# Kernel tuning notes

Measured on AMD Instinct MI355X. Metric: run time of the kernel, lower is better.

The kernel has to match this reference:

```python
import jax, jax.numpy as jnp
import numpy as np

B, L, DM, H, M = 4, 2048, 1024, 16, 256
D = DM // H
CHUNK = 128  # chunk size for exact chunked causal linear attention
KERNEL_EPS = 1e-4
NORM_STAB = 1e-6


def setup_inputs() -> dict:
    key = jax.random.key(0)
    ks = jax.random.split(key, 12)
    n = lambda k, shape, s=1.0: jax.random.normal(k, shape, jnp.float32) * s
    w = DM ** -0.5
    return {
        "q": n(ks[0], (B, L, DM)),
        "k": n(ks[1], (B, L, DM)),
        "v": n(ks[2], (B, L, DM)),
        "Wq": n(ks[3], (DM, DM), w), "bq": n(ks[4], (DM,), 0.01),
        "Wk": n(ks[5], (DM, DM), w), "bk": n(ks[6], (DM,), 0.01),
        "Wv": n(ks[7], (DM, DM), w), "bv": n(ks[8], (DM,), 0.01),
        "Wo": n(ks[9], (DM, DM), w), "bo": n(ks[10], (DM,), 0.01),
        "random_features": n(ks[11], (D, M)),  # projection matrix per head-dim
    }


def performer_forward(q, k, v, Wq, bq, Wk, bk, Wv, bv, Wo, bo, random_features):
    b, l, dm = q.shape
    d, m = random_features.shape
    h = dm // d

    def heads(x, W, bias):
        return (x @ W + bias).reshape(b, l, h, d).transpose(0, 2, 1, 3)  # b h l d

    qh, kh, vh = heads(q, Wq, bq), heads(k, Wk, bk), heads(v, Wv, bv)

    scale = dm ** 0.25
    qs, ksc = qh / scale, kh / scale
    pq = jnp.einsum('bhld,dm->bhlm', qs, random_features)
    pk = jnp.einsum('bhld,dm->bhlm', ksc, random_features)
    hk = -0.5 * jnp.sum(ksc * ksc, axis=-1, keepdims=True)
    k_stab = jnp.max(hk)
    c = m ** -0.5
    # q_stabilizer == h_of_q elementwise (last dim is size 1), so exp(h_q + pq - h_q) = exp(pq)
    qp = c * (jnp.exp(pq) + KERNEL_EPS)                 # b h l m
    kp = c * (jnp.exp(hk + pk - k_stab) + KERNEL_EPS)   # b h l m

    # Exact chunked causal linear attention == cumsum of k'(x)v outer products.
    C = CHUNK
    N = l // C
    qc = qp.reshape(b, h, N, C, m)
    kc = kp.reshape(b, h, N, C, m)
    vc = vh.reshape(b, h, N, C, d)
    tril = jnp.tril(jnp.ones((C, C), dtype=qp.dtype))
    A = jnp.einsum('bhnim,bhnjm->bhnij', qc, kc) * tril           # intra-chunk causal scores
    Ssum = jnp.einsum('bhnjm,bhnjd->bhnmd', kc, vc)               # per-chunk sum of k'(x)v
    Sprev = jnp.cumsum(Ssum, axis=2) - Ssum                       # exclusive prefix over chunks
    num = (jnp.einsum('bhnij,bhnjd->bhnid', A, vc)
           + jnp.einsum('bhnim,bhnmd->bhnid', qc, Sprev))         # b h n C d
    zsum = kc.sum(axis=3)                                         # b h n m
    zprev = jnp.cumsum(zsum, axis=2) - zsum
    den = A.sum(axis=-1) + jnp.einsum('bhnim,bhnm->bhni', qc, zprev)
    den = den + 2.0 * NORM_STAB * (jnp.abs(den) <= NORM_STAB).astype(den.dtype)

    out = (num / den[..., None]).reshape(b, h, l, d)
    ctx = out.transpose(0, 2, 1, 3).reshape(b, l, dm)             # b l (h d)
    return ctx @ Wo + bo


def reference(q, k, v, Wq, bq, Wk, bk, Wv, bv, Wo, bo, random_features):
    return performer_forward(q, k, v, Wq, bq, Wk, bk, Wv, bv, Wo, bo, random_features)
```

## Files before the change

kernel.cpp:

```cpp
#include <hip/hip_runtime.h>


typedef unsigned short u16;
typedef unsigned int u32;
typedef __attribute__((ext_vector_type(8))) short bf16x8;
typedef __attribute__((ext_vector_type(4))) float f32x4;

#define MFMA(a, b, c) __builtin_amdgcn_mfma_f32_16x16x32_bf16(a, b, c, 0, 0, 0)
#define WS_NEED 95420416ull

__device__ __forceinline__ float bf2f(u16 u) { return __uint_as_float(((u32)u) << 16); }
__device__ __forceinline__ u16 f2bf(float f) {
  u32 i = __float_as_uint(f);
  u32 r = i + 0x7FFFu + ((i >> 16) & 1u);
  return (u16)(r >> 16);
}
__device__ __forceinline__ u32 fkey(float x) {
  u32 b = __float_as_uint(x);
  return (b & 0x80000000u) ? ~b : (b | 0x80000000u);
}
__device__ __forceinline__ float unfkey(u32 k) {
  return (k & 0x80000000u) ? __uint_as_float(k & 0x7FFFFFFFu) : __uint_as_float(~k);
}
__device__ __forceinline__ uint4 pack_u16x8(const u16 s[8]) {
  uint4 q;
  q.x = (u32)s[0] | ((u32)s[1] << 16);
  q.y = (u32)s[2] | ((u32)s[3] << 16);
  q.z = (u32)s[4] | ((u32)s[5] << 16);
  q.w = (u32)s[6] | ((u32)s[7] << 16);
  return q;
}
__device__ __forceinline__ void gl_lds16(const u16* g, u16* l) {
  __builtin_amdgcn_global_load_lds((const __attribute__((address_space(1))) unsigned int*)g,
                                   (__attribute__((address_space(3))) unsigned int*)l, 16, 0, 0);
}

__global__ __launch_bounds__(256) void k_cast(const float* __restrict__ src,
                                              u16* __restrict__ dst, int n8) {
  int idx = blockIdx.x * 256 + threadIdx.x;
  if (idx >= n8) return;
  const float4* s = (const float4*)src;
  float4 t0 = s[(size_t)idx * 2], t1 = s[(size_t)idx * 2 + 1];
  u16 p[8] = {f2bf(t0.x), f2bf(t0.y), f2bf(t0.z), f2bf(t0.w),
              f2bf(t1.x), f2bf(t1.y), f2bf(t1.z), f2bf(t1.w)};
  *(uint4*)&dst[(size_t)idx * 8] = pack_u16x8(p);
}

__global__ __launch_bounds__(256) void k_transpose(const float* __restrict__ src,
                                                   u16* __restrict__ dst, int R, int C) {
  __shared__ u16 t[64 * 65];
  int r0 = blockIdx.y * 64, c0 = blockIdx.x * 64;
  for (int i = threadIdx.x; i < 4096; i += 256) {
    int rr = i >> 6, cc = i & 63;
    t[rr * 65 + cc] = f2bf(src[(size_t)(r0 + rr) * C + c0 + cc]);
  }
  __syncthreads();
  for (int i = threadIdx.x; i < 4096; i += 256) {
    int cc = i >> 6, rr = i & 63;
    dst[(size_t)(c0 + cc) * R + r0 + rr] = t[rr * 65 + cc];
  }
}

__global__ void k_init(u32* kstab) { *kstab = fkey(-1e30f); }

__global__ __launch_bounds__(256) void k_guard(float* __restrict__ out, size_t ws_size, int n) {
  if (ws_size >= WS_NEED) return;
  int idx = blockIdx.x * 256 + threadIdx.x;
  if (idx < n) out[idx] = 10000.0f + (float)(ws_size >> 20);
}

__global__ __launch_bounds__(256) void k_proj(const void* __restrict__ X,
                                              const u16* __restrict__ WT,
                                              const float* __restrict__ bias,
                                              void* __restrict__ dst, float* __restrict__ HK,
                                              u32* __restrict__ kstab, int mode) {
  __shared__ __align__(16) u16 As[128 * 64];
  __shared__ __align__(16) u16 Bs[128 * 64];
  const int tid = threadIdx.x;
  const int w = tid >> 6, lane = tid & 63, quad = lane >> 4, l15 = lane & 15;
  const int wr = w >> 1, wc = w & 1;
  const int row0 = blockIdx.y * 128;
  const int n0 = blockIdx.x * 128;
  const int lr = lane >> 3;
  const int sub = lane & 7;
  const int colo = ((sub ^ lr) << 3);
  const u16* Xb = (const u16*)X;
  const int bb3 = row0 >> 11, l03 = row0 & 2047;
  f32x4 acc[4][4] = {};
  for (int kb = 0; kb < 1024; kb += 64) {
    __syncthreads();
#pragma unroll
    for (int i = 0; i < 4; ++i)
      gl_lds16(&WT[(size_t)(n0 + w * 32 + i * 8 + lr) * 1024 + kb + colo],
               &Bs[(w * 4 + i) * 512]);
    if (mode <= 2) {
#pragma unroll
      for (int i = 0; i < 4; ++i)
        gl_lds16(&Xb[(size_t)(row0 + w * 32 + i * 8 + lr) * 1024 + kb + colo],
                 &As[(w * 4 + i) * 512]);
    } else {
      const int hh = kb >> 6;
#pragma unroll
      for (int i = 0; i < 4; ++i)
        gl_lds16(&Xb[(((size_t)bb3 * 16 + hh) * 2048 + l03 + w * 32 + i * 8 + lr) * 64 + colo],
                 &As[(w * 4 + i) * 512]);
    }
    __syncthreads();
#pragma unroll
    for (int kk = 0; kk < 2; ++kk) {
      const int s2 = ((kk * 4 + quad) ^ (l15 & 7)) << 3;
      bf16x8 a[4], b[4];
#pragma unroll
      for (int rt = 0; rt < 4; ++rt)
        a[rt] = *(const bf16x8*)&As[(wr * 64 + rt * 16 + l15) * 64 + s2];
#pragma unroll
      for (int ct = 0; ct < 4; ++ct)
        b[ct] = *(const bf16x8*)&Bs[(wc * 64 + ct * 16 + l15) * 64 + s2];
#pragma unroll
      for (int rt = 0; rt < 4; ++rt)
#pragma unroll
        for (int ct = 0; ct < 4; ++ct) acc[rt][ct] = MFMA(a[rt], b[ct], acc[rt][ct]);
    }
  }
  const float sinv = 0.17677669529663687f;
  const int h = blockIdx.x * 2 + wc;
  float sq[4][4] = {};
#pragma unroll
  for (int rt = 0; rt < 4; ++rt)
#pragma unroll
    for (int ct = 0; ct < 4; ++ct) {
      int col = wc * 64 + ct * 16 + l15;
      float bv = bias[n0 + col];
#pragma unroll
      for (int r = 0; r < 4; ++r) {
        int gr = row0 + wr * 64 + rt * 16 + quad * 4 + r;
        float vv = acc[rt][ct][r] + bv;
        if (mode <= 1) vv *= sinv;
        if (mode == 1) sq[rt][r] += vv * vv;
        if (mode == 3) {
          ((float*)dst)[(size_t)gr * 1024 + n0 + col] = vv;
        } else {
          int bb = gr >> 11, ll = gr & 2047;
          ((u16*)dst)[(((size_t)bb * 16 + h) * 2048 + ll) * 64 + ct * 16 + l15] = f2bf(vv);
        }
      }
    }
  if (mode == 1) {
    float mx = -3.4e38f;
#pragma unroll
    for (int rt = 0; rt < 4; ++rt)
#pragma unroll
      for (int r = 0; r < 4; ++r) {
        float s = sq[rt][r];
        s += __shfl_xor(s, 1);
        s += __shfl_xor(s, 2);
        s += __shfl_xor(s, 4);
        s += __shfl_xor(s, 8);
        float hkv = -0.5f * s;
        if (l15 == 0) {
          int gr = row0 + wr * 64 + rt * 16 + quad * 4 + r;
          int bb = gr >> 11, ll = gr & 2047;
          HK[((size_t)bb * 16 + h) * 2048 + ll] = hkv;
        }
        mx = fmaxf(mx, hkv);
      }
    mx = fmaxf(mx, __shfl_xor(mx, 16));
    mx = fmaxf(mx, __shfl_xor(mx, 32));
    if (lane == 0) atomicMax(kstab, fkey(mx));
  }
}

__global__ __launch_bounds__(256) void k_chunksum(const u16* __restrict__ KS,
                                                  const u16* __restrict__ VH,
                                                  const u16* __restrict__ RFt,
                                                  const float* __restrict__ HK,
                                                  const u32* __restrict__ kstab,
                                                  u16* __restrict__ SS,
                                                  float* __restrict__ ZS) {
  __shared__ __align__(16) u16 smem[22784];
  float* hk_l = (float*)&smem[22016];
  float* zpart = (float*)&smem[22272];
  const int tid = threadIdx.x;
  const int w = tid >> 6, lane = tid & 63, quad = lane >> 4, l15 = lane & 15;
  const int bhn = blockIdx.x, bh = bhn >> 4, n = bhn & 15;
  const u16* kc = KS + (size_t)bhn * 8192;
  const u16* vc = VH + (size_t)bhn * 8192;
  const float kst = unfkey(*kstab);
#pragma unroll
  for (int i = 0; i < 4; ++i) {
    int v = tid + i * 256;
    int rr = v >> 3, c8 = (v & 7) << 3;
    *(uint4*)&smem[rr * 72 + c8] = *(const uint4*)&kc[(size_t)rr * 64 + c8];
  }
  {
    int d = tid & 63, jg = tid >> 6;
#pragma unroll
    for (int g = 0; g < 4; ++g) {
      int j0 = jg * 32 + g * 8;
      u16 s[8];
#pragma unroll
      for (int e = 0; e < 8; ++e) s[e] = vc[(size_t)(j0 + e) * 64 + d];
      *(uint4*)&smem[13312 + d * 136 + j0] = pack_u16x8(s);
    }
  }
  if (tid < 128) hk_l[tid] = HK[(size_t)bh * 2048 + n * 128 + tid];
  __syncthreads();
  bf16x8 ak[2][2];
#pragma unroll
  for (int rt = 0; rt < 2; ++rt)
#pragma unroll
    for (int kk = 0; kk < 2; ++kk)
      ak[rt][kk] = *(const bf16x8*)&smem[(w * 32 + rt * 16 + l15) * 72 + kk * 32 + quad * 8];
  for (int mfb = 0; mfb < 4; ++mfb) {
    __syncthreads();
#pragma unroll
    for (int i = 0; i < 2; ++i) {
      int v = tid + i * 256;
      int rr = v >> 3, c8 = (v & 7) << 3;
      *(uint4*)&smem[rr * 72 + c8] = *(const uint4*)&RFt[(size_t)(mfb * 64 + rr) * 64 + c8];
    }
    __syncthreads();
    f32x4 fk[2][4] = {};
#pragma unroll
    for (int kk = 0; kk < 2; ++kk) {
      bf16x8 rb[4];
#pragma unroll
      for (int ct = 0; ct < 4; ++ct)
        rb[ct] = *(const bf16x8*)&smem[(ct * 16 + l15) * 72 + kk * 32 + quad * 8];
#pragma unroll
      for (int rt = 0; rt < 2; ++rt)
#pragma unroll
        for (int ct = 0; ct < 4; ++ct) fk[rt][ct] = MFMA(ak[rt][kk], rb[ct], fk[rt][ct]);
    }
    float zp4[4] = {0.f, 0.f, 0.f, 0.f};
#pragma unroll
    for (int rt = 0; rt < 2; ++rt)
#pragma unroll
      for (int ct = 0; ct < 4; ++ct) {
        int ml = ct * 16 + l15;
#pragma unroll
        for (int r = 0; r < 4; ++r) {
          int j = w * 32 + rt * 16 + quad * 4 + r;
          float kv = 0.0625f * (expf(fminf(hk_l[j] + fk[rt][ct][r] - kst, 80.f)) + 1e-4f);
          smem[4608 + ml * 136 + j] = f2bf(kv);
          zp4[ct] += kv;
        }
      }
#pragma unroll
    for (int ct = 0; ct < 4; ++ct) {
      float s = zp4[ct];
      s += __shfl_xor(s, 16);
      s += __shfl_xor(s, 32);
      if (quad == 0) zpart[w * 64 + ct * 16 + l15] = s;
    }
    __syncthreads();
    f32x4 acc[4] = {};
#pragma unroll
    for (int kk4 = 0; kk4 < 4; ++kk4) {
      bf16x8 bK = *(const bf16x8*)&smem[4608 + (w * 16 + l15) * 136 + kk4 * 32 + quad * 8];
#pragma unroll
      for (int dt = 0; dt < 4; ++dt) {
        bf16x8 aV = *(const bf16x8*)&smem[13312 + (dt * 16 + l15) * 136 + kk4 * 32 + quad * 8];
        acc[dt] = MFMA(aV, bK, acc[dt]);
      }
    }
#pragma unroll
    for (int dt = 0; dt < 4; ++dt)
#pragma unroll
      for (int r = 0; r < 4; ++r) {
        int d = dt * 16 + quad * 4 + r;
        int mf = mfb * 64 + w * 16 + l15;
        SS[((size_t)bhn * 64 + d) * 256 + mf] = f2bf(acc[dt][r]);
      }
    if (tid < 64) {
      float s = zpart[tid] + zpart[64 + tid] + zpart[128 + tid] + zpart[192 + tid];
      ZS[(size_t)bhn * 256 + mfb * 64 + tid] = s;
    }
  }
}

__global__ __launch_bounds__(256) void k_prefix(u16* __restrict__ SSP,
                                                const float* __restrict__ ZS,
                                                float* __restrict__ ZP) {
  const int bh = blockIdx.x >> 2, dg = blockIdx.x & 3;
  const int tid = threadIdx.x;
  float run[16];
#pragma unroll
  for (int i = 0; i < 16; ++i) run[i] = 0.f;
  for (int n = 0; n < 16; ++n) {
    size_t cb = ((size_t)bh * 16 + n) * 16384 + dg * 4096 + tid;
#pragma unroll
    for (int i = 0; i < 16; ++i) {
      size_t idx = cb + (size_t)i * 256;
      float s = bf2f(SSP[idx]);
      SSP[idx] = f2bf(run[i]);
      run[i] += s;
    }
  }
  if (dg == 0) {
    float zr = 0.f;
    for (int n = 0; n < 16; ++n) {
      size_t zi = ((size_t)bh * 16 + n) * 256 + tid;
      float s = ZS[zi];
      ZP[zi] = zr;
      zr += s;
    }
  }
}

__global__ __launch_bounds__(256) void k_chunkout(const u16* __restrict__ QS,
                                                  const u16* __restrict__ KS,
                                                  const u16* __restrict__ VH,
                                                  const u16* __restrict__ SP,
                                                  const float* __restrict__ ZP,
                                                  const u16* __restrict__ RFt,
                                                  const float* __restrict__ HK,
                                                  const u32* __restrict__ kstab,
                                                  u16* __restrict__ CTX) {
  __shared__ __align__(16) u16 smem[28160];
  float* hk_l = (float*)&smem[27648];
  float* den_l = (float*)&smem[27904];
  const int tid = threadIdx.x;
  const int w = tid >> 6, lane = tid & 63, quad = lane >> 4, l15 = lane & 15;
  const int bhn = blockIdx.x, bh = bhn >> 4, n = bhn & 15;
  const u16* qc = QS + (size_t)bhn * 8192;
  const u16* kc = KS + (size_t)bhn * 8192;
  const u16* vc = VH + (size_t)bhn * 8192;
  const u16* sp = SP + (size_t)bhn * 16384;
  const float* zp = ZP + (size_t)bhn * 256;
  const float kst = unfkey(*kstab);
#pragma unroll
  for (int i = 0; i < 4; ++i) {
    int v = tid + i * 256;
    int rr = v >> 3, c8 = (v & 7) << 3;
    *(uint4*)&smem[rr * 72 + c8] = *(const uint4*)&qc[(size_t)rr * 64 + c8];
    *(uint4*)&smem[9216 + rr * 72 + c8] = *(const uint4*)&kc[(size_t)rr * 64 + c8];
  }
  if (tid < 128) hk_l[tid] = HK[(size_t)bh * 2048 + n * 128 + tid];
  __syncthreads();
  bf16x8 aq[2][2], ak[2][2];
#pragma unroll
  for (int rt = 0; rt < 2; ++rt)
#pragma unroll
    for (int kk = 0; kk < 2; ++kk) {
      aq[rt][kk] = *(const bf16x8*)&smem[(w * 32 + rt * 16 + l15) * 72 + kk * 32 + quad * 8];
      ak[rt][kk] =
          *(const bf16x8*)&smem[9216 + (w * 32 + rt * 16 + l15) * 72 + kk * 32 + quad * 8];
    }
  f32x4 sc[2][8] = {};
  f32x4 nm[2][4] = {};
  float den2p[2][4] = {};
  for (int mfb = 0; mfb < 4; ++mfb) {
    __syncthreads();
#pragma unroll
    for (int i = 0; i < 2; ++i) {
      int v = tid + i * 256;
      int rr = v >> 3, c8 = (v & 7) << 3;
      *(uint4*)&smem[rr * 72 + c8] = *(const uint4*)&RFt[(size_t)(mfb * 64 + rr) * 64 + c8];
      *(uint4*)&smem[23040 + rr * 72 + c8] = *(const uint4*)&sp[(size_t)rr * 256 + mfb * 64 + c8];
    }
    __syncthreads();
    f32x4 fq[2][4] = {}, fk[2][4] = {};
#pragma unroll
    for (int kk = 0; kk < 2; ++kk) {
      bf16x8 rb[4];
#pragma unroll
      for (int ct = 0; ct < 4; ++ct)
        rb[ct] = *(const bf16x8*)&smem[(ct * 16 + l15) * 72 + kk * 32 + quad * 8];
#pragma unroll
      for (int rt = 0; rt < 2; ++rt)
#pragma unroll
        for (int ct = 0; ct < 4; ++ct) {
          fq[rt][ct] = MFMA(aq[rt][kk], rb[ct], fq[rt][ct]);
          fk[rt][ct] = MFMA(ak[rt][kk], rb[ct], fk[rt][ct]);
        }
    }
#pragma unroll
    for (int ct = 0; ct < 4; ++ct) {
      int ml = ct * 16 + l15;
      float zpv = zp[mfb * 64 + ml];
#pragma unroll
      for (int rt = 0; rt < 2; ++rt)
#pragma unroll
        for (int r = 0; r < 4; ++r) {
          int row = w * 32 + rt * 16 + quad * 4 + r;
          float qv = 0.0625f * (expf(fminf(fq[rt][ct][r], 80.f)) + 1e-4f);
          smem[4608 + row * 72 + ml] = f2bf(qv);
          den2p[rt][r] += qv * zpv;
          float kv = 0.0625f * (expf(fminf(hk_l[row] + fk[rt][ct][r] - kst, 80.f)) + 1e-4f);
          smem[13824 + row * 72 + ml] = f2bf(kv);
        }
    }
    __syncthreads();
#pragma unroll
    for (int kk = 0; kk < 2; ++kk) {
      bf16x8 aqp[2];
#pragma unroll
      for (int rt = 0; rt < 2; ++rt)
        aqp[rt] =
            *(const bf16x8*)&smem[4608 + (w * 32 + rt * 16 + l15) * 72 + kk * 32 + quad * 8];
      bf16x8 bk8[8];
#pragma unroll
      for (int ct = 0; ct < 8; ++ct)
        bk8[ct] = *(const bf16x8*)&smem[13824 + (ct * 16 + l15) * 72 + kk * 32 + quad * 8];
      bf16x8 bs4[4];
#pragma unroll
      for (int c4 = 0; c4 < 4; ++c4)
        bs4[c4] = *(const bf16x8*)&smem[23040 + (c4 * 16 + l15) * 72 + kk * 32 + quad * 8];
#pragma unroll
      for (int rt = 0; rt < 2; ++rt) {
#pragma unroll
        for (int ct = 0; ct < 8; ++ct) sc[rt][ct] = MFMA(aqp[rt], bk8[ct], sc[rt][ct]);
#pragma unroll
        for (int c4 = 0; c4 < 4; ++c4) nm[rt][c4] = MFMA(aqp[rt], bs4[c4], nm[rt][c4]);
      }
    }
  }
  __syncthreads();
#pragma unroll
  for (int rt = 0; rt < 2; ++rt)
#pragma unroll
    for (int r = 0; r < 4; ++r) {
      float s = den2p[rt][r];
      s += __shfl_xor(s, 1);
      s += __shfl_xor(s, 2);
      s += __shfl_xor(s, 4);
      s += __shfl_xor(s, 8);
      if (l15 == 0) den_l[w * 32 + rt * 16 + quad * 4 + r] = s;
    }
  float rs[2][4] = {};
#pragma unroll
  for (int rt = 0; rt < 2; ++rt)
#pragma unroll
    for (int ct = 0; ct < 8; ++ct)
#pragma unroll
      for (int r = 0; r < 4; ++r) {
        int i = w * 32 + rt * 16 + quad * 4 + r;
        int j = ct * 16 + l15;
        float vv = (j <= i) ? sc[rt][ct][r] : 0.f;
        rs[rt][r] += vv;
        smem[i * 136 + j] = f2bf(vv);
      }
#pragma unroll
  for (int rt = 0; rt < 2; ++rt)
#pragma unroll
    for (int r = 0; r < 4; ++r) {
      float s = rs[rt][r];
      s += __shfl_xor(s, 1);
      s += __shfl_xor(s, 2);
      s += __shfl_xor(s, 4);
      s += __shfl_xor(s, 8);
      if (l15 == 0) den_l[w * 32 + rt * 16 + quad * 4 + r] += s;
    }
  {
    int d = tid & 63, jg = tid >> 6;
#pragma unroll
    for (int g = 0; g < 4; ++g) {
      int j0 = jg * 32 + g * 8;
      u16 s[8];
#pragma unroll
      for (int e = 0; e < 8; ++e) s[e] = vc[(size_t)(j0 + e) * 64 + d];
      *(uint4*)&smem[17408 + d * 136 + j0] = pack_u16x8(s);
    }
  }
  __syncthreads();
#pragma unroll
  for (int kk4 = 0; kk4 < 4; ++kk4) {
    bf16x8 aA[2];
#pragma unroll
    for (int rt = 0; rt < 2; ++rt)
      aA[rt] = *(const bf16x8*)&smem[(w * 32 + rt * 16 + l15) * 136 + kk4 * 32 + quad * 8];
    bf16x8 bv4[4];
#pragma unroll
    for (int c4 = 0; c4 < 4; ++c4)
      bv4[c4] = *(const bf16x8*)&smem[17408 + (c4 * 16 + l15) * 136 + kk4 * 32 + quad * 8];
#pragma unroll
    for (int rt = 0; rt < 2; ++rt)
#pragma unroll
      for (int c4 = 0; c4 < 4; ++c4) nm[rt][c4] = MFMA(aA[rt], bv4[c4], nm[rt][c4]);
  }
  if (tid < 128) {
    float dv = den_l[tid];
    if (fabsf(dv) <= 1e-6f) dv += 2e-6f;
    den_l[tid] = dv;
  }
  __syncthreads();
#pragma unroll
  for (int rt = 0; rt < 2; ++rt)
#pragma unroll
    for (int c4 = 0; c4 < 4; ++c4)
#pragma unroll
      for (int r = 0; r < 4; ++r) {
        int i = w * 32 + rt * 16 + quad * 4 + r;
        int d = c4 * 16 + l15;
        float o = nm[rt][c4][r] / den_l[i];
        CTX[(size_t)bhn * 8192 + (size_t)i * 64 + d] = f2bf(o);
      }
}

extern "C" void kernel_launch(void* const* d_in, const int* in_sizes, int n_in,
                              void* d_out, int out_size, void* d_ws, size_t ws_size,
                              hipStream_t stream) {
  const float* q = (const float*)d_in[0];
  const float* k = (const float*)d_in[1];
  const float* v = (const float*)d_in[2];
  const float* Wq = (const float*)d_in[3];
  const float* bq = (const float*)d_in[4];
  const float* Wk = (const float*)d_in[5];
  const float* bk = (const float*)d_in[6];
  const float* Wv = (const float*)d_in[7];
  const float* bv = (const float*)d_in[8];
  const float* Wo = (const float*)d_in[9];
  const float* bo = (const float*)d_in[10];
  const float* RF = (const float*)d_in[11];
  char* W = (char*)d_ws;
  u16* WqT = (u16*)(W + 0);
  u16* WkT = (u16*)(W + 2097152);
  u16* WvT = (u16*)(W + 4194304);
  u16* WoT = (u16*)(W + 6291456);
  u16* RFt = (u16*)(W + 8388608);
  u32* KSTAB = (u32*)(W + 8421376);
  float* HK = (float*)(W + 8421632);
  float* ZS = (float*)(W + 8945920);
  float* ZP = (float*)(W + 9994496);
  u16* QS = (u16*)(W + 11534336);
  u16* KS = (u16*)(W + 28311552);
  u16* VH = (u16*)(W + 45088768);
  u16* SS = (u16*)(W + 61865984);
  u16* XB = SS;
  u16* CTX = QS;

  k_transpose<<<dim3(16, 16), 256, 0, stream>>>(Wq, WqT, 1024, 1024);
  k_transpose<<<dim3(16, 16), 256, 0, stream>>>(Wk, WkT, 1024, 1024);
  k_transpose<<<dim3(16, 16), 256, 0, stream>>>(Wv, WvT, 1024, 1024);
  k_transpose<<<dim3(16, 16), 256, 0, stream>>>(Wo, WoT, 1024, 1024);
  k_transpose<<<dim3(4, 1), 256, 0, stream>>>(RF, RFt, 64, 256);
  k_init<<<1, 1, 0, stream>>>(KSTAB);
  k_cast<<<4096, 256, 0, stream>>>(q, XB, 1048576);
  k_proj<<<dim3(8, 64), 256, 0, stream>>>(XB, WqT, bq, QS, HK, KSTAB, 0);
  k_cast<<<4096, 256, 0, stream>>>(k, XB, 1048576);
  k_proj<<<dim3(8, 64), 256, 0, stream>>>(XB, WkT, bk, KS, HK, KSTAB, 1);
  k_cast<<<4096, 256, 0, stream>>>(v, XB, 1048576);
  k_proj<<<dim3(8, 64), 256, 0, stream>>>(XB, WvT, bv, VH, HK, KSTAB, 2);
  k_chunksum<<<1024, 256, 0, stream>>>(KS, VH, RFt, HK, KSTAB, SS, ZS);
  k_prefix<<<256, 256, 0, stream>>>(SS, ZS, ZP);
  k_chunkout<<<1024, 256, 0, stream>>>(QS, KS, VH, SS, ZP, RFt, HK, KSTAB, CTX);
  k_proj<<<dim3(8, 64), 256, 0, stream>>>(CTX, WoT, bo, d_out, HK, KSTAB, 3);
  k_guard<<<32768, 256, 0, stream>>>((float*)d_out, ws_size, out_size);
  (void)in_sizes; (void)n_in;
}
```

Baseline: 489.5 us.

## Merge weight transposes, widen prefix grid, swizzle LDS, fast exp, occupancy hints

```diff
diff --git a/kernel.cpp b/kernel.cpp
--- a/kernel.cpp
+++ b/kernel.cpp
@@ -44,6 +44,27 @@
   u16 p[8] = {f2bf(t0.x), f2bf(t0.y), f2bf(t0.z), f2bf(t0.w),
               f2bf(t1.x), f2bf(t1.y), f2bf(t1.z), f2bf(t1.w)};
   *(uint4*)&dst[(size_t)idx * 8] = pack_u16x8(p);
+}
+
+__global__ __launch_bounds__(256) void k_transpose4(const float* __restrict__ s0,
+                                                    const float* __restrict__ s1,
+                                                    const float* __restrict__ s2,
+                                                    const float* __restrict__ s3,
+                                                    u16* __restrict__ d0, u16* __restrict__ d1,
+                                                    u16* __restrict__ d2, u16* __restrict__ d3) {
+  __shared__ u16 t[64 * 65];
+  const float* src = (blockIdx.z == 0) ? s0 : (blockIdx.z == 1) ? s1 : (blockIdx.z == 2) ? s2 : s3;
+  u16* dst = (blockIdx.z == 0) ? d0 : (blockIdx.z == 1) ? d1 : (blockIdx.z == 2) ? d2 : d3;
+  int r0 = blockIdx.y * 64, c0 = blockIdx.x * 64;
+  for (int i = threadIdx.x; i < 4096; i += 256) {
+    int rr = i >> 6, cc = i & 63;
+    t[rr * 65 + cc] = f2bf(src[(size_t)(r0 + rr) * 1024 + c0 + cc]);
+  }
+  __syncthreads();
+  for (int i = threadIdx.x; i < 4096; i += 256) {
+    int cc = i >> 6, rr = i & 63;
+    dst[(size_t)(c0 + cc) * 1024 + r0 + rr] = t[rr * 65 + cc];
+  }
 }
 
 __global__ __launch_bounds__(256) void k_transpose(const float* __restrict__ src,
@@ -170,13 +191,13 @@
   }
 }
 
-__global__ __launch_bounds__(256) void k_chunksum(const u16* __restrict__ KS,
-                                                  const u16* __restrict__ VH,
-                                                  const u16* __restrict__ RFt,
-                                                  const float* __restrict__ HK,
-                                                  const u32* __restrict__ kstab,
-                                                  u16* __restrict__ SS,
-                                                  float* __restrict__ ZS) {
+__global__ __launch_bounds__(256, 3) void k_chunksum(const u16* __restrict__ KS,
+                                                     const u16* __restrict__ VH,
+                                                     const u16* __restrict__ RFt,
+                                                     const float* __restrict__ HK,
+                                                     const u32* __restrict__ kstab,
+                                                     u16* __restrict__ SS,
+                                                     float* __restrict__ ZS) {
   __shared__ __align__(16) u16 smem[22784];
   float* hk_l = (float*)&smem[22016];
   float* zpart = (float*)&smem[22272];
@@ -241,7 +262,7 @@
 #pragma unroll
         for (int r = 0; r < 4; ++r) {
           int j = w * 32 + rt * 16 + quad * 4 + r;
-          float kv = 0.0625f * (expf(fminf(hk_l[j] + fk[rt][ct][r] - kst, 80.f)) + 1e-4f);
+          float kv = 0.0625f * (__expf(fminf(hk_l[j] + fk[rt][ct][r] - kst, 80.f)) + 1e-4f);
           smem[4608 + ml * 136 + j] = f2bf(kv);
           zp4[ct] += kv;
         }
@@ -282,22 +303,20 @@
 __global__ __launch_bounds__(256) void k_prefix(u16* __restrict__ SSP,
                                                 const float* __restrict__ ZS,
                                                 float* __restrict__ ZP) {
-  const int bh = blockIdx.x >> 2, dg = blockIdx.x & 3;
+  const int dgg = blockIdx.x, bh = blockIdx.y;
   const int tid = threadIdx.x;
-  float run[16];
-#pragma unroll
-  for (int i = 0; i < 16; ++i) run[i] = 0.f;
+  float run[4] = {0.f, 0.f, 0.f, 0.f};
   for (int n = 0; n < 16; ++n) {
-    size_t cb = ((size_t)bh * 16 + n) * 16384 + dg * 4096 + tid;
-#pragma unroll
-    for (int i = 0; i < 16; ++i) {
+    size_t cb = ((size_t)bh * 16 + n) * 16384 + (size_t)dgg * 1024 + tid;
+#pragma unroll
+    for (int i = 0; i < 4; ++i) {
       size_t idx = cb + (size_t)i * 256;
       float s = bf2f(SSP[idx]);
       SSP[idx] = f2bf(run[i]);
       run[i] += s;
     }
   }
-  if (dg == 0) {
+  if (dgg == 0) {
     float zr = 0.f;
     for (int n = 0; n < 16; ++n) {
       size_t zi = ((size_t)bh * 16 + n) * 256 + tid;
@@ -308,18 +327,18 @@
   }
 }
 
-__global__ __launch_bounds__(256) void k_chunkout(const u16* __restrict__ QS,
-                                                  const u16* __restrict__ KS,
-                                                  const u16* __restrict__ VH,
-                                                  const u16* __restrict__ SP,
-                                                  const float* __restrict__ ZP,
-                                                  const u16* __restrict__ RFt,
-                                                  const float* __restrict__ HK,
-                                                  const u32* __restrict__ kstab,
-                                                  u16* __restrict__ CTX) {
-  __shared__ __align__(16) u16 smem[28160];
-  float* hk_l = (float*)&smem[27648];
-  float* den_l = (float*)&smem[27904];
+__global__ __launch_bounds__(256, 3) void k_chunkout(const u16* __restrict__ QS,
+                                                     const u16* __restrict__ KS,
+                                                     const u16* __restrict__ VH,
+                                                     const u16* __restrict__ SP,
+                                                     const float* __restrict__ ZP,
+                                                     const u16* __restrict__ RFt,
+                                                     const float* __restrict__ HK,
+                                                     const u32* __restrict__ kstab,
+                                                     u16* __restrict__ CTX) {
+  __shared__ __align__(16) u16 smem[27136];
+  float* hk_l = (float*)&smem[26624];
+  float* den_l = (float*)&smem[26880];
   const int tid = threadIdx.x;
   const int w = tid >> 6, lane = tid & 63, quad = lane >> 4, l15 = lane & 15;
   const int bhn = blockIdx.x, bh = bhn >> 4, n = bhn & 15;
@@ -355,9 +374,11 @@
 #pragma unroll
     for (int i = 0; i < 2; ++i) {
       int v = tid + i * 256;
-      int rr = v >> 3, c8 = (v & 7) << 3;
-      *(uint4*)&smem[rr * 72 + c8] = *(const uint4*)&RFt[(size_t)(mfb * 64 + rr) * 64 + c8];
-      *(uint4*)&smem[23040 + rr * 72 + c8] = *(const uint4*)&sp[(size_t)rr * 256 + mfb * 64 + c8];
+      int rr = v >> 3, cc = v & 7;
+      int sw = ((cc ^ (rr & 7)) << 3);
+      *(uint4*)&smem[rr * 64 + sw] = *(const uint4*)&RFt[(size_t)(mfb * 64 + rr) * 64 + (cc << 3)];
+      *(uint4*)&smem[22528 + rr * 64 + sw] =
+          *(const uint4*)&sp[(size_t)rr * 256 + mfb * 64 + (cc << 3)];
     }
     __syncthreads();
     f32x4 fq[2][4] = {}, fk[2][4] = {};
@@ -366,7 +387,7 @@
       bf16x8 rb[4];
 #pragma unroll
       for (int ct = 0; ct < 4; ++ct)
-        rb[ct] = *(const bf16x8*)&smem[(ct * 16 + l15) * 72 + kk * 32 + quad * 8];
+        rb[ct] = *(const bf16x8*)&smem[(ct * 16 + l15) * 64 + (((kk * 4 + quad) ^ (l15 & 7)) << 3)];
 #pragma unroll
       for (int rt = 0; rt < 2; ++rt)
 #pragma unroll
@@ -384,11 +405,11 @@
 #pragma unroll
         for (int r = 0; r < 4; ++r) {
           int row = w * 32 + rt * 16 + quad * 4 + r;
-          float qv = 0.0625f * (expf(fminf(fq[rt][ct][r], 80.f)) + 1e-4f);
-          smem[4608 + row * 72 + ml] = f2bf(qv);
+          float qv = 0.0625f * (__expf(fminf(fq[rt][ct][r], 80.f)) + 1e-4f);
+          smem[4096 + row * 72 + ml] = f2bf(qv);
           den2p[rt][r] += qv * zpv;
-          float kv = 0.0625f * (expf(fminf(hk_l[row] + fk[rt][ct][r] - kst, 80.f)) + 1e-4f);
-          smem[13824 + row * 72 + ml] = f2bf(kv);
+          float kv = 0.0625f * (__expf(fminf(hk_l[row] + fk[rt][ct][r] - kst, 80.f)) + 1e-4f);
+          smem[13312 + row * 72 + ml] = f2bf(kv);
         }
     }
     __syncthreads();
@@ -398,15 +419,16 @@
 #pragma unroll
       for (int rt = 0; rt < 2; ++rt)
         aqp[rt] =
-            *(const bf16x8*)&smem[4608 + (w * 32 + rt * 16 + l15) * 72 + kk * 32 + quad * 8];
+            *(const bf16x8*)&smem[4096 + (w * 32 + rt * 16 + l15) * 72 + kk * 32 + quad * 8];
       bf16x8 bk8[8];
 #pragma unroll
       for (int ct = 0; ct < 8; ++ct)
-        bk8[ct] = *(const bf16x8*)&smem[13824 + (ct * 16 + l15) * 72 + kk * 32 + quad * 8];
+        bk8[ct] = *(const bf16x8*)&smem[13312 + (ct * 16 + l15) * 72 + kk * 32 + quad * 8];
       bf16x8 bs4[4];
 #pragma unroll
       for (int c4 = 0; c4 < 4; ++c4)
-        bs4[c4] = *(const bf16x8*)&smem[23040 + (c4 * 16 + l15) * 72 + kk * 32 + quad * 8];
+        bs4[c4] = *(const bf16x8*)&smem[22528 + (c4 * 16 + l15) * 64 +
+                                        (((kk * 4 + quad) ^ (l15 & 7)) << 3)];
 #pragma unroll
       for (int rt = 0; rt < 2; ++rt) {
 #pragma unroll
@@ -530,10 +552,7 @@
   u16* XB = SS;
   u16* CTX = QS;
 
-  k_transpose<<<dim3(16, 16), 256, 0, stream>>>(Wq, WqT, 1024, 1024);
-  k_transpose<<<dim3(16, 16), 256, 0, stream>>>(Wk, WkT, 1024, 1024);
-  k_transpose<<<dim3(16, 16), 256, 0, stream>>>(Wv, WvT, 1024, 1024);
-  k_transpose<<<dim3(16, 16), 256, 0, stream>>>(Wo, WoT, 1024, 1024);
+  k_transpose4<<<dim3(16, 16, 4), 256, 0, stream>>>(Wq, Wk, Wv, Wo, WqT, WkT, WvT, WoT);
   k_transpose<<<dim3(4, 1), 256, 0, stream>>>(RF, RFt, 64, 256);
   k_init<<<1, 1, 0, stream>>>(KSTAB);
   k_cast<<<4096, 256, 0, stream>>>(q, XB, 1048576);
@@ -543,7 +562,7 @@
   k_cast<<<4096, 256, 0, stream>>>(v, XB, 1048576);
   k_proj<<<dim3(8, 64), 256, 0, stream>>>(XB, WvT, bv, VH, HK, KSTAB, 2);
   k_chunksum<<<1024, 256, 0, stream>>>(KS, VH, RFt, HK, KSTAB, SS, ZS);
-  k_prefix<<<256, 256, 0, stream>>>(SS, ZS, ZP);
+  k_prefix<<<dim3(16, 64), 256, 0, stream>>>(SS, ZS, ZP);
   k_chunkout<<<1024, 256, 0, stream>>>(QS, KS, VH, SS, ZP, RFt, HK, KSTAB, CTX);
   k_proj<<<dim3(8, 64), 256, 0, stream>>>(CTX, WoT, bo, d_out, HK, KSTAB, 3);
   k_guard<<<32768, 256, 0, stream>>>((float*)d_out, ws_size, out_size);
```

After: 501.9 us. +2.5%, slower.
